# Kernel optimization log

Measured on AMD Instinct MI355X. Metric: run time of the kernel, lower is better.

Reference implementation:

```python
import jax, jax.numpy as jnp
import numpy as np
import math

B, S, L, H, NH, FF, V = 32, 512, 12, 768, 12, 3072, 30522
DH = H // NH


def setup_inputs() -> dict:
    key = jax.random.key(0)
    ks = jax.random.split(key, 16)
    w = lambda k, shape: (jax.random.normal(k, shape, jnp.float32) * 0.02)
    return {
        "input_ids": jax.random.randint(ks[0], (B, S), 0, V, dtype=jnp.int32),
        "attention_mask": jax.random.uniform(ks[1], (B, S), jnp.float32),
        "word_emb": w(ks[2], (V, H)),
        "pos_emb": w(ks[3], (S, H)),
        "type_emb": w(ks[4], (H,)),
        "ln_emb_s": jnp.ones((H,), jnp.float32),
        "ln_emb_b": jnp.zeros((H,), jnp.float32),
        "Wq": w(ks[5], (L, H, H)), "bq": jnp.zeros((L, H), jnp.float32),
        "Wk": w(ks[6], (L, H, H)), "bk": jnp.zeros((L, H), jnp.float32),
        "Wv": w(ks[7], (L, H, H)), "bv": jnp.zeros((L, H), jnp.float32),
        "Wo": w(ks[8], (L, H, H)), "bo": jnp.zeros((L, H), jnp.float32),
        "ln1_s": jnp.ones((L, H), jnp.float32), "ln1_b": jnp.zeros((L, H), jnp.float32),
        "Wi": w(ks[9], (L, H, FF)), "bi": jnp.zeros((L, FF), jnp.float32),
        "Wf": w(ks[10], (L, FF, H)), "bf": jnp.zeros((L, H), jnp.float32),
        "ln2_s": jnp.ones((L, H), jnp.float32), "ln2_b": jnp.zeros((L, H), jnp.float32),
    }


def _ln(x, s, b):
    # BERT LayerNorm, eps=1e-12
    m = jnp.mean(x, -1, keepdims=True)
    v = jnp.mean((x - m) ** 2, -1, keepdims=True)
    return (x - m) * jax.lax.rsqrt(v + 1e-12) * s + b


def reference(input_ids, attention_mask, word_emb, pos_emb, type_emb,
              ln_emb_s, ln_emb_b, Wq, bq, Wk, bk, Wv, bv, Wo, bo,
              ln1_s, ln1_b, Wi, bi, Wf, bf, ln2_s, ln2_b):
    b, s = input_ids.shape
    scale = 1.0 / math.sqrt(DH)
    # Embeddings: word + position + (single) token-type, then LayerNorm
    h = word_emb[input_ids] + pos_emb[None, :s] + type_emb
    h = _ln(h, ln_emb_s, ln_emb_b)
    key_mask = attention_mask[:, None, None, :]  # [B,1,1,S], float

    def layer(h, p):
        wq, bq_, wk, bk_, wv, bv_, wo, bo_, l1s, l1b, wi, bi_, wf, bf_, l2s, l2b = p
        q = (jnp.einsum('bsd,de->bse', h, wq) + bq_).reshape(b, s, NH, DH)
        k = (jnp.einsum('bsd,de->bse', h, wk) + bk_).reshape(b, s, NH, DH)
        v = (jnp.einsum('bsd,de->bse', h, wv) + bv_).reshape(b, s, NH, DH)
        scores = jnp.einsum('bqhd,bkhd->bhqk', q, k) * scale
        probs = jax.nn.softmax(scores, axis=-1)
        # post-softmax masking + renormalization (the non-standard part)
        probs = probs * key_mask
        probs = probs / jnp.clip(jnp.sum(probs, -1, keepdims=True), 1e-9, None)
        ctx = jnp.einsum('bhqk,bkhd->bqhd', probs, v).reshape(b, s, H)
        attn_out = _ln(jnp.einsum('bsd,de->bse', ctx, wo) + bo_ + h, l1s, l1b)
        inter = jax.nn.gelu(jnp.einsum('bsd,df->bsf', attn_out, wi) + bi_, approximate=False)
        out = _ln(jnp.einsum('bsf,fd->bsd', inter, wf) + bf_ + attn_out, l2s, l2b)
        return out, None

    h, _ = jax.lax.scan(layer, h, (Wq, bq, Wk, bk, Wv, bv, Wo, bo,
                                   ln1_s, ln1_b, Wi, bi, Wf, bf, ln2_s, ln2_b))
    # masked mean pooling + L2 normalize (normalize=True)
    m = attention_mask[..., None]
    sent = jnp.sum(h * m, axis=1) / jnp.clip(jnp.sum(m, axis=1), 1e-6, None)
    sent = sent / jnp.clip(jnp.linalg.norm(sent, axis=-1, keepdims=True), 1e-12, None)
    return sent
```

## Files before the change

### kernel.cpp

```cpp
#include <hip/hip_runtime.h>
#include <hip/hip_bf16.h>
#include <math.h>

typedef __bf16 bf16;
typedef __bf16 bf16x8 __attribute__((ext_vector_type(8)));
typedef float  f32x4  __attribute__((ext_vector_type(4)));

#define B_  32
#define S_  512
#define H_  768
#define NH_ 12
#define DH_ 64
#define FF_ 3072
#define L_  12
#define M_  (B_*S_)
#define QKV_ 2304

#define VST 516
#define PST 68

__device__ __forceinline__ void gload16(const bf16* g, bf16* l) {
  __builtin_amdgcn_global_load_lds(
      (const __attribute__((address_space(1))) void*)g,
      (__attribute__((address_space(3))) void*)l, 16, 0, 0);
}

__device__ __forceinline__ float fast_gelu(float x) {
  float z = x * 0.70710678118f;
  float s = fabsf(z);
  float t = __builtin_amdgcn_rcpf(1.0f + 0.3275911f * s);
  float p = t*(0.254829592f + t*(-0.284496736f + t*(1.421413741f +
            t*(-1.453152027f + t*1.061405429f))));
  float e = p * __expf(-s*s);
  float erfv = copysignf(1.0f - e, z);
  return 0.5f * x * (1.0f + erfv);
}

__global__ __launch_bounds__(512, 4) void gemm128(
    const bf16* __restrict__ A, const bf16* __restrict__ Bt,
    const float* __restrict__ bias, void* __restrict__ outp,
    int N, int K, int tiles_n, int epi)
{
  __shared__ bf16 As[128*64];
  __shared__ bf16 Bs[128*64];
  const int tid  = threadIdx.x;
  const int lane = tid & 63, wid = tid >> 6;
  const int wr = wid >> 2, wc = wid & 3;
  const int lrow = lane & 15, kgrp = lane >> 4;

  const int nwg = gridDim.x, orig = blockIdx.x;
  const int qc = nwg >> 3, rc = nwg & 7;
  const int xcd = orig & 7, lin = orig >> 3;
  const int wg = (xcd < rc ? xcd*(qc+1) : rc*(qc+1) + (xcd-rc)*qc) + lin;
  const int tm = wg / tiles_n, tn = wg % tiles_n;
  const size_t m0 = (size_t)tm * 128, n0 = (size_t)tn * 128;
  const int KT = K >> 6;

  const bf16* Ab = A  + m0 * K;
  const bf16* Bb = Bt + n0 * K;

  auto stage = [&](const bf16* gbase, bf16* ldsbase, int kt) {
#pragma unroll
    for (int j = 0; j < 2; ++j) {
      int lin2  = j*512 + tid;
      int prow  = lin2 >> 3;
      int pslot = lin2 & 7;
      int lslot = pslot ^ (prow & 7);
      const bf16* src = gbase + (size_t)prow * K + (size_t)kt*64 + lslot*8;
      bf16* dst = ldsbase + (size_t)(j*512 + (wid<<6))*8;
      gload16(src, dst);
    }
  };

  f32x4 acc[4][2] = {};

  for (int t = 0; t < KT; ++t) {
    __syncthreads();
    stage(Ab, As, t);
    stage(Bb, Bs, t);
    __syncthreads();
#pragma unroll
    for (int kk = 0; kk < 2; ++kk) {
      bf16x8 a[4], b[2];
#pragma unroll
      for (int m = 0; m < 4; ++m) {
        int row  = wr*64 + m*16 + lrow;
        int slot = (kk*4 + kgrp) ^ (lrow & 7);
        a[m] = *(const bf16x8*)&As[row*64 + slot*8];
      }
#pragma unroll
      for (int n = 0; n < 2; ++n) {
        int row  = wc*32 + n*16 + lrow;
        int slot = (kk*4 + kgrp) ^ (lrow & 7);
        b[n] = *(const bf16x8*)&Bs[row*64 + slot*8];
      }
#pragma unroll
      for (int m = 0; m < 4; ++m)
#pragma unroll
        for (int n = 0; n < 2; ++n)
          acc[m][n] = __builtin_amdgcn_mfma_f32_16x16x32_bf16(a[m], b[n], acc[m][n], 0, 0, 0);
    }
  }

#pragma unroll
  for (int m = 0; m < 4; ++m)
#pragma unroll
    for (int n = 0; n < 2; ++n) {
      int col = (int)n0 + wc*32 + n*16 + lrow;
      float bv = bias[col];
#pragma unroll
      for (int r = 0; r < 4; ++r) {
        int row = (int)m0 + wr*64 + m*16 + kgrp*4 + r;
        float x = acc[m][n][r] + bv;
        size_t idx = (size_t)row * N + col;
        if (epi == 1)      ((float*)outp)[idx] = x;
        else if (epi == 0) ((bf16*)outp)[idx]  = (bf16)x;
        else               ((bf16*)outp)[idx]  = (bf16)fast_gelu(x);
      }
    }
}

__global__ __launch_bounds__(256) void weight_prep(
    const float* __restrict__ Wq, const float* __restrict__ Wk,
    const float* __restrict__ Wv, const float* __restrict__ Wo,
    const float* __restrict__ Wi, const float* __restrict__ Wf,
    const float* __restrict__ bq, const float* __restrict__ bk,
    const float* __restrict__ bv,
    bf16* __restrict__ wqkv, bf16* __restrict__ wot,
    bf16* __restrict__ wit,  bf16* __restrict__ wft,
    float* __restrict__ qkbias)
{
  int bid = blockIdx.x;
  if (bid >= 1728) {
    int i = (bid - 1728)*256 + threadIdx.x;
    if (i < QKV_)
      qkbias[i] = (i < 768) ? bq[i] : (i < 1536 ? bk[i-768] : bv[i-1536]);
    return;
  }
  const float* W; bf16* Wt; int K, N, t;
  if (bid < 576) {
    K = 768; N = 768;
    if      (bid < 144) { W = Wq; Wt = wqkv;             t = bid; }
    else if (bid < 288) { W = Wk; Wt = wqkv + 768*768;   t = bid - 144; }
    else if (bid < 432) { W = Wv; Wt = wqkv + 2*768*768; t = bid - 288; }
    else                { W = Wo; Wt = wot;              t = bid - 432; }
  } else if (bid < 1152) { W = Wi; Wt = wit; K = 768;  N = 3072; t = bid - 576; }
  else                   { W = Wf; Wt = wft; K = 3072; N = 768;  t = bid - 1152; }
  const int kt = K >> 6;
  const int k0 = (t % kt)*64, n0 = (t / kt)*64;

  __shared__ bf16 T[64][65];
  int tx = threadIdx.x & 63, ty = threadIdx.x >> 6;
#pragma unroll
  for (int j = 0; j < 16; ++j) {
    int kk = j*4 + ty;
    T[kk][tx] = (bf16)W[(size_t)(k0+kk)*N + n0 + tx];
  }
  __syncthreads();
#pragma unroll
  for (int j = 0; j < 16; ++j) {
    int nn = j*4 + ty;
    Wt[(size_t)(n0+nn)*K + k0 + tx] = T[tx][nn];
  }
}

__device__ __forceinline__ void block_sum2(float& a, float& b, float* red) {
  int lane = threadIdx.x & 63, wid = threadIdx.x >> 6;
  for (int o = 32; o > 0; o >>= 1) { a += __shfl_xor(a, o); b += __shfl_xor(b, o); }
  if (lane == 0) { red[wid*2] = a; red[wid*2+1] = b; }
  __syncthreads();
  a = red[0] + red[2] + red[4] + red[6];
  b = red[1] + red[3] + red[5] + red[7];
  __syncthreads();
}

__global__ __launch_bounds__(256) void embed_ln(
    const int* __restrict__ ids, const float* __restrict__ we,
    const float* __restrict__ pe, const float* __restrict__ te,
    const float* __restrict__ gs, const float* __restrict__ gb,
    float* __restrict__ h32, bf16* __restrict__ hb)
{
  __shared__ float red[8];
  int row = blockIdx.x;
  int s = row & (S_-1);
  int id = ids[row];
  int t = threadIdx.x;
  float x[3], sum = 0.f, sq = 0.f;
#pragma unroll
  for (int j = 0; j < 3; ++j) {
    int c = t + j*256;
    float v = we[(size_t)id*H_ + c] + pe[(size_t)s*H_ + c] + te[c];
    x[j] = v; sum += v; sq += v*v;
  }
  block_sum2(sum, sq, red);
  float mean = sum * (1.f/H_);
  float var  = sq  * (1.f/H_) - mean*mean;
  float rstd = rsqrtf(fmaxf(var, 0.f) + 1e-12f);
#pragma unroll
  for (int j = 0; j < 3; ++j) {
    int c = t + j*256;
    float y = (x[j]-mean)*rstd*gs[c] + gb[c];
    h32[(size_t)row*H_ + c] = y;
    hb [(size_t)row*H_ + c] = (bf16)y;
  }
}

__global__ __launch_bounds__(256) void ln_res(
    const bf16* __restrict__ t16, const float* __restrict__ res,
    const float* __restrict__ gs, const float* __restrict__ gb,
    float* __restrict__ o32, bf16* __restrict__ ob)
{
  __shared__ float red[8];
  int row = blockIdx.x, t = threadIdx.x;
  float x[3], sum = 0.f, sq = 0.f;
#pragma unroll
  for (int j = 0; j < 3; ++j) {
    int c = t + j*256;
    float v = (float)t16[(size_t)row*H_ + c] + res[(size_t)row*H_ + c];
    x[j] = v; sum += v; sq += v*v;
  }
  block_sum2(sum, sq, red);
  float mean = sum * (1.f/H_);
  float var  = sq  * (1.f/H_) - mean*mean;
  float rstd = rsqrtf(fmaxf(var, 0.f) + 1e-12f);
#pragma unroll
  for (int j = 0; j < 3; ++j) {
    int c = t + j*256;
    float y = (x[j]-mean)*rstd*gs[c] + gb[c];
    o32[(size_t)row*H_ + c] = y;
    ob [(size_t)row*H_ + c] = (bf16)y;
  }
}

__global__ __launch_bounds__(512, 2) void attn_kernel(
    const bf16* __restrict__ qkv, const float* __restrict__ mask,
    bf16* __restrict__ ctx)
{
  __shared__ bf16 Kl[S_*64];
  __shared__ bf16 Vt[DH_*VST];
  __shared__ float mk[S_];
  __shared__ bf16 Pl[8][16*PST];
  int tid = threadIdx.x, lane = tid & 63, wid = tid >> 6;
  int lrow = lane & 15, kgrp = lane >> 4;
  int cur_head = -1;

  bf16x8 onesv;
#pragma unroll
  for (int i = 0; i < 8; ++i) onesv[i] = (bf16)1.0f;

  for (int u = 0; u < 6; ++u) {
    int unit = blockIdx.x*6 + u;
    int hh = unit >> 2, pass = unit & 3;
    int b = hh / NH_, h = hh % NH_;
    const bf16* Qb = qkv + (size_t)(b*S_)*QKV_ + h*DH_;

    if (hh != cur_head) {
      __syncthreads();
      const bf16* Kb = qkv + (size_t)(b*S_)*QKV_ + H_   + h*DH_;
      const bf16* Vb = qkv + (size_t)(b*S_)*QKV_ + 2*H_ + h*DH_;
#pragma unroll
      for (int it = 0; it < 8; ++it) {
        int lin   = it*512 + tid;
        int prow  = lin >> 3;
        int pslot = lin & 7;
        int lslot = pslot ^ (prow & 7);
        gload16(&Kb[(size_t)prow*QKV_ + lslot*8],
                &Kl[(size_t)(it*512 + (wid<<6))*8]);
      }
      for (int it = 0; it < 8; ++it) {
        int slot = it*512 + tid;
        int s = slot >> 3, c8 = (slot & 7)*8;
        bf16x8 v = *(const bf16x8*)&Vb[(size_t)s*QKV_ + c8];
#pragma unroll
        for (int i = 0; i < 8; ++i) Vt[(c8+i)*VST + s] = v[i];
      }
      mk[tid] = mask[b*S_ + tid];
      cur_head = hh;
      __syncthreads();
    }

    int q0 = pass*128 + wid*16;
    bf16x8 qa[2];
#pragma unroll
    for (int kc = 0; kc < 2; ++kc) {
      qa[kc] = *(const bf16x8*)&Qb[(size_t)(q0 + lrow)*QKV_ + kc*32 + kgrp*8];
#pragma unroll
      for (int i = 0; i < 8; ++i)
        qa[kc][i] = (bf16)((float)qa[kc][i] * 0.125f);
    }
    f32x4 O[4] = {};
    f32x4 O5 = {};
    float mrun[4];
#pragma unroll
    for (int r = 0; r < 4; ++r) mrun[r] = -1e30f;

#pragma unroll 2
    for (int c0 = 0; c0 < S_; c0 += 64) {
      f32x4 Sf[4] = {};
      __builtin_amdgcn_s_setprio(1);
#pragma unroll
      for (int kc = 0; kc < 2; ++kc)
#pragma unroll
        for (int sn = 0; sn < 4; ++sn) {
          int row  = c0 + sn*16 + lrow;
          int slot = (kc*4 + kgrp) ^ (lrow & 7);
          bf16x8 kbv = *(const bf16x8*)&Kl[(size_t)row*64 + slot*8];
          Sf[sn] = __builtin_amdgcn_mfma_f32_16x16x32_bf16(qa[kc], kbv, Sf[sn], 0, 0, 0);
        }
      __builtin_amdgcn_s_setprio(0);

      float lm[4];
#pragma unroll
      for (int r = 0; r < 4; ++r)
        lm[r] = fmaxf(fmaxf(Sf[0][r], Sf[1][r]), fmaxf(Sf[2][r], Sf[3][r]));
      bool small = (lm[0] <= mrun[0]+8.f) && (lm[1] <= mrun[1]+8.f) &&
                   (lm[2] <= mrun[2]+8.f) && (lm[3] <= mrun[3]+8.f);
      bool skip = __all(small);
      float newm[4];
      if (skip) {
#pragma unroll
        for (int r = 0; r < 4; ++r) newm[r] = mrun[r];
      } else {
        float cmax[4];
#pragma unroll
        for (int r = 0; r < 4; ++r) cmax[r] = lm[r];
        for (int o = 1; o < 16; o <<= 1)
#pragma unroll
          for (int r = 0; r < 4; ++r) cmax[r] = fmaxf(cmax[r], __shfl_xor(cmax[r], o));
#pragma unroll
        for (int r = 0; r < 4; ++r) {
          newm[r] = fmaxf(mrun[r], cmax[r]);
          float fr = __expf(mrun[r] - newm[r]);
#pragma unroll
          for (int on = 0; on < 4; ++on) O[on][r] *= fr;
          O5[r] *= fr;
          mrun[r] = newm[r];
        }
      }
#pragma unroll
      for (int sn = 0; sn < 4; ++sn) {
        float mkv = mk[c0 + sn*16 + lrow];
#pragma unroll
        for (int r = 0; r < 4; ++r) {
          float e = __expf(Sf[sn][r] - newm[r]) * mkv;
          Pl[wid][(kgrp*4 + r)*PST + sn*16 + lrow] = (bf16)e;
        }
      }
      __builtin_amdgcn_s_setprio(1);
#pragma unroll
      for (int kc = 0; kc < 2; ++kc) {
        bf16x8 pa = *(const bf16x8*)&Pl[wid][lrow*PST + kc*32 + kgrp*8];
#pragma unroll
        for (int on = 0; on < 4; ++on) {
          bf16x8 vv = *(const bf16x8*)&Vt[(on*16 + lrow)*VST + c0 + kc*32 + kgrp*8];
          O[on] = __builtin_amdgcn_mfma_f32_16x16x32_bf16(pa, vv, O[on], 0, 0, 0);
        }
        O5 = __builtin_amdgcn_mfma_f32_16x16x32_bf16(pa, onesv, O5, 0, 0, 0);
      }
      __builtin_amdgcn_s_setprio(0);
    }
#pragma unroll
    for (int on = 0; on < 4; ++on)
#pragma unroll
      for (int r = 0; r < 4; ++r) {
        float val = O[on][r] / fmaxf(O5[r], 1e-9f);
        int q = q0 + kgrp*4 + r;
        ctx[(size_t)(b*S_ + q)*H_ + h*DH_ + on*16 + lrow] = (bf16)val;
      }
  }
}

__global__ __launch_bounds__(256) void pool_partial(
    const float* __restrict__ h32, const float* __restrict__ mask,
    float* __restrict__ part)
{
  int b = blockIdx.x >> 3, ch = blockIdx.x & 7;
  int t = threadIdx.x;
  float a0 = 0.f, a1 = 0.f, a2 = 0.f;
  for (int s = ch*64; s < ch*64 + 64; ++s) {
    float m = mask[b*S_ + s];
    const float* hp = &h32[((size_t)b*S_ + s)*H_];
    a0 += hp[t]*m; a1 += hp[t+256]*m; a2 += hp[t+512]*m;
  }
  float* pp = &part[(size_t)(b*8 + ch)*H_];
  pp[t] = a0; pp[t+256] = a1; pp[t+512] = a2;
}

__global__ __launch_bounds__(256) void pool_final(
    const float* __restrict__ part, const float* __restrict__ mask,
    float* __restrict__ out)
{
  __shared__ float red[8];
  int b = blockIdx.x, t = threadIdx.x;
  float s0 = 0.f, s1 = 0.f, s2 = 0.f;
#pragma unroll
  for (int ch = 0; ch < 8; ++ch) {
    const float* pp = &part[(size_t)(b*8 + ch)*H_];
    s0 += pp[t]; s1 += pp[t+256]; s2 += pp[t+512];
  }
  float msum = mask[b*S_ + t] + mask[b*S_ + 256 + t];
  float dummy = 0.f;
  block_sum2(msum, dummy, red);
  float inv = 1.f / fmaxf(msum, 1e-6f);
  s0 *= inv; s1 *= inv; s2 *= inv;
  float nrm = s0*s0 + s1*s1 + s2*s2;
  dummy = 0.f;
  block_sum2(nrm, dummy, red);
  float rn = 1.f / fmaxf(sqrtf(nrm), 1e-12f);
  out[b*H_ + t]       = s0*rn;
  out[b*H_ + t + 256] = s1*rn;
  out[b*H_ + t + 512] = s2*rn;
}

extern "C" void kernel_launch(void* const* d_in, const int* in_sizes, int n_in,
                              void* d_out, int out_size, void* d_ws, size_t ws_size,
                              hipStream_t stream)
{
  const int*   ids  = (const int*)  d_in[0];
  const float* mask = (const float*)d_in[1];
  const float* we   = (const float*)d_in[2];
  const float* pe   = (const float*)d_in[3];
  const float* te   = (const float*)d_in[4];
  const float* les  = (const float*)d_in[5];
  const float* leb  = (const float*)d_in[6];
  const float* Wq   = (const float*)d_in[7];
  const float* bq   = (const float*)d_in[8];
  const float* Wk   = (const float*)d_in[9];
  const float* bk   = (const float*)d_in[10];
  const float* Wv   = (const float*)d_in[11];
  const float* bv   = (const float*)d_in[12];
  const float* Wo   = (const float*)d_in[13];
  const float* bo   = (const float*)d_in[14];
  const float* l1s  = (const float*)d_in[15];
  const float* l1b  = (const float*)d_in[16];
  const float* Wi   = (const float*)d_in[17];
  const float* bi   = (const float*)d_in[18];
  const float* Wf   = (const float*)d_in[19];
  const float* bfp  = (const float*)d_in[20];
  const float* l2s  = (const float*)d_in[21];
  const float* l2b  = (const float*)d_in[22];

  char* p = (char*)d_ws;
  auto alloc = [&](size_t bytes) { char* q = p; p += (bytes + 255) & ~(size_t)255; return q; };
  bf16*  wqkv = (bf16*) alloc((size_t)QKV_*H_*2);
  bf16*  wot  = (bf16*) alloc((size_t)H_*H_*2);
  bf16*  wit  = (bf16*) alloc((size_t)H_*FF_*2);
  bf16*  wft  = (bf16*) alloc((size_t)H_*FF_*2);
  float* qkbias=(float*)alloc((size_t)QKV_*4);
  bf16*  hb   = (bf16*) alloc((size_t)M_*H_*2);
  float* h32  = (float*)alloc((size_t)M_*H_*4);
  float* a32  = (float*)alloc((size_t)M_*H_*4);
  bf16*  tmpb = (bf16*) alloc((size_t)M_*H_*2);
  bf16*  qkvb = (bf16*) alloc((size_t)M_*QKV_*2);
  bf16*  cxb  = (bf16*) alloc((size_t)M_*H_*2);
  bf16*  inb  = (bf16*) alloc((size_t)M_*FF_*2);
  float* part = (float*)alloc((size_t)B_*8*H_*4);

  embed_ln<<<M_, 256, 0, stream>>>(ids, we, pe, te, les, leb, h32, hb);

  for (int l = 0; l < L_; ++l) {
    size_t wsq = (size_t)l*H_*H_;
    weight_prep<<<1737, 256, 0, stream>>>(
        Wq + wsq, Wk + wsq, Wv + wsq, Wo + wsq,
        Wi + (size_t)l*H_*FF_, Wf + (size_t)l*FF_*H_,
        bq + l*H_, bk + l*H_, bv + l*H_,
        wqkv, wot, wit, wft, qkbias);

    gemm128<<<128*(QKV_/128), 512, 0, stream>>>(hb,  wqkv, qkbias,      qkvb, QKV_, H_,  QKV_/128, 0);
    attn_kernel<<<256, 512, 0, stream>>>(qkvb, mask, cxb);
    gemm128<<<128*(H_/128),  512, 0, stream>>>(cxb, wot, bo  + l*H_,  tmpb, H_,  H_,  H_/128,  0);
    ln_res<<<M_, 256, 0, stream>>>(tmpb, h32, l1s + l*H_, l1b + l*H_, a32, hb);
    gemm128<<<128*(FF_/128), 512, 0, stream>>>(hb,  wit, bi  + l*FF_, inb,  FF_, H_,  FF_/128, 2);
    gemm128<<<128*(H_/128),  512, 0, stream>>>(inb, wft, bfp + l*H_,  tmpb, H_,  FF_, H_/128,  0);
    ln_res<<<M_, 256, 0, stream>>>(tmpb, a32, l2s + l*H_, l2b + l*H_, h32, hb);
  }

  pool_partial<<<B_*8, 256, 0, stream>>>(h32, mask, part);
  pool_final<<<B_, 256, 0, stream>>>(part, mask, (float*)d_out);
}
```

Measured before the change: 4.971 ms.

## Keep residual stream in bf16 and process two rows per LayerNorm block

Drops the fp32 copies of the hidden state and attention output, so the residual stream is stored and read only as bf16. LayerNorm kernels now read bf16 residuals with 2-element vector loads, and each block handles two rows, which halves the grid size. Pooling also reads the bf16 hidden state. This reduces memory traffic in the LayerNorm and pooling kernels, but each layer's residual now carries bf16 rounding, which may reduce accuracy.

```diff
diff --git a/kernel.cpp b/kernel.cpp
--- a/kernel.cpp
+++ b/kernel.cpp
@@ -3,6 +3,7 @@
 #include <math.h>
 
 typedef __bf16 bf16;
+typedef __bf16 bf16x2 __attribute__((ext_vector_type(2)));
 typedef __bf16 bf16x8 __attribute__((ext_vector_type(8)));
 typedef float  f32x4  __attribute__((ext_vector_type(4)));
 
@@ -178,7 +179,7 @@
     const int* __restrict__ ids, const float* __restrict__ we,
     const float* __restrict__ pe, const float* __restrict__ te,
     const float* __restrict__ gs, const float* __restrict__ gb,
-    float* __restrict__ h32, bf16* __restrict__ hb)
+    bf16* __restrict__ hb)
 {
   __shared__ float red[8];
   int row = blockIdx.x;
@@ -200,35 +201,49 @@
   for (int j = 0; j < 3; ++j) {
     int c = t + j*256;
     float y = (x[j]-mean)*rstd*gs[c] + gb[c];
-    h32[(size_t)row*H_ + c] = y;
-    hb [(size_t)row*H_ + c] = (bf16)y;
-  }
-}
-
-__global__ __launch_bounds__(256) void ln_res(
-    const bf16* __restrict__ t16, const float* __restrict__ res,
+    hb[(size_t)row*H_ + c] = (bf16)y;
+  }
+}
+
+__global__ __launch_bounds__(256) void ln_res2(
+    const bf16* __restrict__ t16, const bf16* __restrict__ res,
     const float* __restrict__ gs, const float* __restrict__ gb,
-    float* __restrict__ o32, bf16* __restrict__ ob)
-{
-  __shared__ float red[8];
-  int row = blockIdx.x, t = threadIdx.x;
-  float x[3], sum = 0.f, sq = 0.f;
+    bf16* __restrict__ out)
+{
+  __shared__ float red[2][2][2];
+  int t = threadIdx.x;
+  int rloc = t & 127, rsel = t >> 7, wir = (t >> 6) & 1;
+  size_t row = (size_t)blockIdx.x*2 + rsel;
+  const bf16* tp = t16 + row*H_;
+  const bf16* rp = res + row*H_;
+  float x[6];
+  float sum = 0.f, sq = 0.f;
 #pragma unroll
   for (int j = 0; j < 3; ++j) {
-    int c = t + j*256;
-    float v = (float)t16[(size_t)row*H_ + c] + res[(size_t)row*H_ + c];
-    x[j] = v; sum += v; sq += v*v;
-  }
-  block_sum2(sum, sq, red);
+    int c = rloc*2 + j*256;
+    bf16x2 a = *(const bf16x2*)&tp[c];
+    bf16x2 b = *(const bf16x2*)&rp[c];
+    float v0 = (float)a[0] + (float)b[0];
+    float v1 = (float)a[1] + (float)b[1];
+    x[j*2] = v0; x[j*2+1] = v1;
+    sum += v0 + v1; sq += v0*v0 + v1*v1;
+  }
+  for (int o = 32; o > 0; o >>= 1) { sum += __shfl_xor(sum, o); sq += __shfl_xor(sq, o); }
+  if ((t & 63) == 0) { red[rsel][wir][0] = sum; red[rsel][wir][1] = sq; }
+  __syncthreads();
+  sum = red[rsel][0][0] + red[rsel][1][0];
+  sq  = red[rsel][0][1] + red[rsel][1][1];
   float mean = sum * (1.f/H_);
   float var  = sq  * (1.f/H_) - mean*mean;
   float rstd = rsqrtf(fmaxf(var, 0.f) + 1e-12f);
+  bf16* op = out + row*H_;
 #pragma unroll
   for (int j = 0; j < 3; ++j) {
-    int c = t + j*256;
-    float y = (x[j]-mean)*rstd*gs[c] + gb[c];
-    o32[(size_t)row*H_ + c] = y;
-    ob [(size_t)row*H_ + c] = (bf16)y;
+    int c = rloc*2 + j*256;
+    bf16x2 o2;
+    o2[0] = (bf16)((x[j*2]   - mean)*rstd*gs[c]   + gb[c]);
+    o2[1] = (bf16)((x[j*2+1] - mean)*rstd*gs[c+1] + gb[c+1]);
+    *(bf16x2*)&op[c] = o2;
   }
 }
 
@@ -371,7 +386,7 @@
 }
 
 __global__ __launch_bounds__(256) void pool_partial(
-    const float* __restrict__ h32, const float* __restrict__ mask,
+    const bf16* __restrict__ hb, const float* __restrict__ mask,
     float* __restrict__ part)
 {
   int b = blockIdx.x >> 3, ch = blockIdx.x & 7;
@@ -379,8 +394,8 @@
   float a0 = 0.f, a1 = 0.f, a2 = 0.f;
   for (int s = ch*64; s < ch*64 + 64; ++s) {
     float m = mask[b*S_ + s];
-    const float* hp = &h32[((size_t)b*S_ + s)*H_];
-    a0 += hp[t]*m; a1 += hp[t+256]*m; a2 += hp[t+512]*m;
+    const bf16* hp = &hb[((size_t)b*S_ + s)*H_];
+    a0 += (float)hp[t]*m; a1 += (float)hp[t+256]*m; a2 += (float)hp[t+512]*m;
   }
   float* pp = &part[(size_t)(b*8 + ch)*H_];
   pp[t] = a0; pp[t+256] = a1; pp[t+512] = a2;
@@ -448,15 +463,14 @@
   bf16*  wft  = (bf16*) alloc((size_t)H_*FF_*2);
   float* qkbias=(float*)alloc((size_t)QKV_*4);
   bf16*  hb   = (bf16*) alloc((size_t)M_*H_*2);
-  float* h32  = (float*)alloc((size_t)M_*H_*4);
-  float* a32  = (float*)alloc((size_t)M_*H_*4);
+  bf16*  ab   = (bf16*) alloc((size_t)M_*H_*2);
   bf16*  tmpb = (bf16*) alloc((size_t)M_*H_*2);
   bf16*  qkvb = (bf16*) alloc((size_t)M_*QKV_*2);
   bf16*  cxb  = (bf16*) alloc((size_t)M_*H_*2);
   bf16*  inb  = (bf16*) alloc((size_t)M_*FF_*2);
   float* part = (float*)alloc((size_t)B_*8*H_*4);
 
-  embed_ln<<<M_, 256, 0, stream>>>(ids, we, pe, te, les, leb, h32, hb);
+  embed_ln<<<M_, 256, 0, stream>>>(ids, we, pe, te, les, leb, hb);
 
   for (int l = 0; l < L_; ++l) {
     size_t wsq = (size_t)l*H_*H_;
@@ -469,12 +483,12 @@
     gemm128<<<128*(QKV_/128), 512, 0, stream>>>(hb,  wqkv, qkbias,      qkvb, QKV_, H_,  QKV_/128, 0);
     attn_kernel<<<256, 512, 0, stream>>>(qkvb, mask, cxb);
     gemm128<<<128*(H_/128),  512, 0, stream>>>(cxb, wot, bo  + l*H_,  tmpb, H_,  H_,  H_/128,  0);
-    ln_res<<<M_, 256, 0, stream>>>(tmpb, h32, l1s + l*H_, l1b + l*H_, a32, hb);
-    gemm128<<<128*(FF_/128), 512, 0, stream>>>(hb,  wit, bi  + l*FF_, inb,  FF_, H_,  FF_/128, 2);
+    ln_res2<<<M_/2, 256, 0, stream>>>(tmpb, hb, l1s + l*H_, l1b + l*H_, ab);
+    gemm128<<<128*(FF_/128), 512, 0, stream>>>(ab,  wit, bi  + l*FF_, inb,  FF_, H_,  FF_/128, 2);
     gemm128<<<128*(H_/128),  512, 0, stream>>>(inb, wft, bfp + l*H_,  tmpb, H_,  FF_, H_/128,  0);
-    ln_res<<<M_, 256, 0, stream>>>(tmpb, a32, l2s + l*H_, l2b + l*H_, h32, hb);
-  }
-
-  pool_partial<<<B_*8, 256, 0, stream>>>(h32, mask, part);
+    ln_res2<<<M_/2, 256, 0, stream>>>(tmpb, ab, l2s + l*H_, l2b + l*H_, hb);
+  }
+
+  pool_partial<<<B_*8, 256, 0, stream>>>(hb, mask, part);
   pool_final<<<B_, 256, 0, stream>>>(part, mask, (float*)d_out);
 }
```

After: 4.698 ms (median of 2 runs). 1.06x faster.
